# Optimization experiments

Measured on AMD Instinct MI355X. Metric: run time of the kernel, lower is better.

The kernel has to match this reference:

```python
import jax, jax.numpy as jnp
import numpy as np
import math

# dims: batch, seq_len, d_model, heads, head_dim
B, L, DM, H, DH = 1, 4096, 1024, 16, 64
BS, W, MAXD, DFF = 64, 16, 256, 4096  # block_size, band width (blocks), max rel distance, ffn dim
NB = L // BS


def _static_layout():
    # Static block-sparse causal band layout: tgt block n attends to src blocks [n-W+1 .. n].
    # Mirrors construct_blocksparse_rel_ids: rel = tgt_pos - src_pos, pos ids start at 1
    # (0 reserved for padding), clamp rel<-1 -> -1, rel>max_distance -> max_distance, then +1.
    n = np.arange(NB)[:, None, None, None]
    w = np.arange(W)[None, :, None, None]
    i = np.arange(BS)[None, None, :, None]
    j = np.arange(BS)[None, None, None, :]
    src_blk = n - (W - 1) + w
    # valid: block exists; diagonal block (w==W-1) is causal within-block (j<=i)
    valid = (src_blk >= 0) & ((w < W - 1) | (j <= i))
    tgt_pos = n * BS + i + 1
    src_pos = np.clip(src_blk, 0, None) * BS + j + 1
    rel = np.clip(tgt_pos - src_pos, -1, MAXD) + 1
    rel = np.where(valid, rel, 0)  # masked positions get rel id 0 (as in masked_fill_)
    src_idx = np.clip(np.arange(NB)[:, None] - (W - 1) + np.arange(W)[None, :], 0, None)
    return jnp.asarray(rel), jnp.asarray(valid), jnp.asarray(src_idx)

REL_IDS, VALID, SRC_IDX = _static_layout()  # [NB,W,BS,BS], [NB,W,BS,BS], [NB,W]


def _ln(x, g, b):
    m = x.mean(-1, keepdims=True)
    v = ((x - m) ** 2).mean(-1, keepdims=True)
    return (x - m) * jax.lax.rsqrt(v + 1e-5) * g + b


def setup_inputs() -> dict:
    key = jax.random.key(0)
    ks = jax.random.split(key, 10)
    p = lambda k, shape: jax.random.normal(k, shape, jnp.float32) * 0.02
    return dict(
        x=jax.random.normal(ks[0], (B, L, DM), jnp.float32),
        Wq=p(ks[1], (DM, DM)), Wk=p(ks[2], (DM, DM)), Wv=p(ks[3], (DM, DM)),
        Wo=p(ks[4], (DM, DM)),
        rel_emb=p(ks[5], (MAXD + 2, H)),  # per-head relative position bias table
        ln1_g=jnp.ones((DM,), jnp.float32), ln1_b=jnp.zeros((DM,), jnp.float32),
        ln2_g=jnp.ones((DM,), jnp.float32), ln2_b=jnp.zeros((DM,), jnp.float32),
        W1=p(ks[6], (DM, DFF)), b1=jnp.zeros((DFF,), jnp.float32),
        W2=p(ks[7], (DFF, DM)), b2=jnp.zeros((DM,), jnp.float32),
    )


def reference(x, Wq, Wk, Wv, Wo, rel_emb, ln1_g, ln1_b, ln2_g, ln2_b, W1, b1, W2, b2):
    h = _ln(x, ln1_g, ln1_b)

    def heads(Wt):
        return (h @ Wt).reshape(B, NB, BS, H, DH).transpose(0, 3, 1, 2, 4)  # [B,H,NB,BS,DH]

    q, k, v = heads(Wq), heads(Wk), heads(Wv)
    k_band = k[:, :, SRC_IDX]  # gather nonzero src blocks -> [B,H,NB,W,BS,DH]
    v_band = v[:, :, SRC_IDX]
    scores = jnp.einsum('bhnid,bhnwjd->bhniwj', q, k_band) / math.sqrt(DH)
    # relative position bias, per block pair and head
    bias = rel_emb[REL_IDS].transpose(4, 0, 2, 1, 3)  # [H,NB,BS,W,BS]
    scores = scores + bias[None]
    mask = VALID.transpose(0, 2, 1, 3)  # [NB,BS,W,BS]
    scores = jnp.where(mask, scores, jnp.float32(-1e30))
    p = jax.nn.softmax(scores.reshape(B, H, NB, BS, W * BS), axis=-1)
    p = p.reshape(B, H, NB, BS, W, BS)
    o = jnp.einsum('bhniwj,bhnwjd->bhnid', p, v_band)
    o = o.transpose(0, 2, 3, 1, 4).reshape(B, L, DM) @ Wo
    x = x + o
    h2 = _ln(x, ln2_g, ln2_b)
    x = x + (jax.nn.gelu(h2 @ W1 + b1) @ W2 + b2)
    return x
```

## Files before the change

kernel.cpp:

```cpp
#include <hip/hip_runtime.h>
#include <math.h>

typedef __bf16 bf16x8 __attribute__((ext_vector_type(8)));
typedef float  f32x4  __attribute__((ext_vector_type(4)));
typedef short  s16x8  __attribute__((ext_vector_type(8)));

__device__ __forceinline__ unsigned short f2bf(float f) {
    unsigned int u = __float_as_uint(f);
    u += 0x7fffu + ((u >> 16) & 1u);
    return (unsigned short)(u >> 16);
}

__device__ __forceinline__ float gelu_tanh(float x) {
    float x3 = x * x * x;
    float t = tanhf(0.7978845608028654f * (x + 0.044715f * x3));
    return 0.5f * x * (1.0f + t);
}

__global__ __launch_bounds__(256) void tcvt_kernel(const float* __restrict__ in,
                                                   unsigned short* __restrict__ out,
                                                   int K, int N) {
    __shared__ float tile[32][33];
    int tx = threadIdx.x, ty = threadIdx.y;
    int k0 = blockIdx.y * 32, n0 = blockIdx.x * 32;
#pragma unroll
    for (int s = 0; s < 4; ++s)
        tile[ty + s * 8][tx] = in[(size_t)(k0 + ty + s * 8) * N + n0 + tx];
    __syncthreads();
#pragma unroll
    for (int s = 0; s < 4; ++s)
        out[(size_t)(n0 + ty + s * 8) * K + k0 + tx] = f2bf(tile[tx][ty + s * 8]);
}

__global__ __launch_bounds__(256) void ln_kernel(const float* __restrict__ x,
                                                 const float* __restrict__ g,
                                                 const float* __restrict__ b,
                                                 unsigned short* __restrict__ out) {
    int row = blockIdx.x;
    int tid = threadIdx.x;
    float4 v = ((const float4*)(x + (size_t)row * 1024))[tid];
    float s  = v.x + v.y + v.z + v.w;
    float ss = v.x * v.x + v.y * v.y + v.z * v.z + v.w * v.w;
#pragma unroll
    for (int o = 32; o > 0; o >>= 1) { s += __shfl_down(s, o); ss += __shfl_down(ss, o); }
    __shared__ float red[8];
    if ((tid & 63) == 0) { red[(tid >> 6) * 2] = s; red[(tid >> 6) * 2 + 1] = ss; }
    __syncthreads();
    s  = red[0] + red[2] + red[4] + red[6];
    ss = red[1] + red[3] + red[5] + red[7];
    float mean = s * (1.0f / 1024.0f);
    float var  = ss * (1.0f / 1024.0f) - mean * mean;
    float rs   = rsqrtf(var + 1e-5f);
    float4 gv = ((const float4*)g)[tid];
    float4 bv = ((const float4*)b)[tid];
    ushort4 o4;
    o4.x = f2bf((v.x - mean) * rs * gv.x + bv.x);
    o4.y = f2bf((v.y - mean) * rs * gv.y + bv.y);
    o4.z = f2bf((v.z - mean) * rs * gv.z + bv.z);
    o4.w = f2bf((v.w - mean) * rs * gv.w + bv.w);
    ((ushort4*)(out + (size_t)row * 1024))[tid] = o4;
}

__global__ __launch_bounds__(256) void tvt_kernel(const unsigned short* __restrict__ in,
                                                  unsigned short* __restrict__ out) {
    __shared__ unsigned short tile[64][72];
    int t = threadIdx.x;
    int l0 = blockIdx.x * 64, c0 = blockIdx.y * 64;
    int tr = t >> 3, tc = (t & 7) * 8;
#pragma unroll
    for (int s = 0; s < 2; ++s) {
        int r = tr + s * 32;
        s16x8 v = *(const s16x8*)(in + (size_t)(l0 + r) * 3072 + 2048 + c0 + tc);
        *(s16x8*)(&tile[r][tc]) = v;
    }
    __syncthreads();
#pragma unroll
    for (int s = 0; s < 2; ++s) {
        int c = tr + s * 32;
        s16x8 w;
#pragma unroll
        for (int e = 0; e < 8; ++e) w[e] = (short)tile[tc + e][c];
        *(s16x8*)(out + (size_t)(c0 + c) * 4096 + l0 + tc) = w;
    }
}

#define BM 128
#define BN 128
#define BKK 64

template <int EPI>
__global__ __launch_bounds__(256) void gemm_kernel(const unsigned short* __restrict__ A,
                                                   const unsigned short* __restrict__ Bt,
                                                   void* __restrict__ C,
                                                   const float* __restrict__ bias,
                                                   const float* __restrict__ resid,
                                                   int M, int N, int K) {
    __shared__ __align__(16) unsigned short sA[BM * BKK];
    __shared__ __align__(16) unsigned short sB[BN * BKK];

    const int tid  = threadIdx.x;
    const int wv   = tid >> 6;
    const int lane = tid & 63;
    const int wr   = wv >> 1, wc = wv & 1;
    const int lg   = lane >> 4;
    const int l15  = lane & 15;

    const int brow = blockIdx.y * BM;
    const int bcol = blockIdx.x * BN;

    f32x4 acc[4][4] = {};

    const int l8 = lane >> 3;
    const int lc = (lane & 7) * 8;

    for (int kt = 0; kt < K; kt += BKK) {
        __syncthreads();
#pragma unroll
        for (int q = 0; q < 4; ++q) {
            int ch = 4 * wv + q;
            const unsigned short* srcA = A + (size_t)(brow + 8 * ch + l8) * K + kt + lc;
            __builtin_amdgcn_global_load_lds((const __attribute__((address_space(1))) void*)srcA,
                                             (__attribute__((address_space(3))) void*)(sA + ch * 512),
                                             16, 0, 0);
        }
#pragma unroll
        for (int q = 0; q < 4; ++q) {
            int ch = 4 * wv + q;
            const unsigned short* srcB = Bt + (size_t)(bcol + 8 * ch + l8) * K + kt + lc;
            __builtin_amdgcn_global_load_lds((const __attribute__((address_space(1))) void*)srcB,
                                             (__attribute__((address_space(3))) void*)(sB + ch * 512),
                                             16, 0, 0);
        }
        __syncthreads();

        bf16x8 af[4][2], bfr[4][2];
#pragma unroll
        for (int mi = 0; mi < 4; ++mi)
#pragma unroll
            for (int kk = 0; kk < 2; ++kk)
                af[mi][kk] = *(const bf16x8*)(sA + (wr * 64 + mi * 16 + l15) * BKK + lg * 8 + kk * 32);
#pragma unroll
        for (int ni = 0; ni < 4; ++ni)
#pragma unroll
            for (int kk = 0; kk < 2; ++kk)
                bfr[ni][kk] = *(const bf16x8*)(sB + (wc * 64 + ni * 16 + l15) * BKK + lg * 8 + kk * 32);

#pragma unroll
        for (int kk = 0; kk < 2; ++kk)
#pragma unroll
            for (int mi = 0; mi < 4; ++mi)
#pragma unroll
                for (int ni = 0; ni < 4; ++ni)
                    acc[mi][ni] = __builtin_amdgcn_mfma_f32_16x16x32_bf16(af[mi][kk], bfr[ni][kk],
                                                                          acc[mi][ni], 0, 0, 0);
    }

#pragma unroll
    for (int mi = 0; mi < 4; ++mi)
#pragma unroll
        for (int ni = 0; ni < 4; ++ni)
#pragma unroll
            for (int r = 0; r < 4; ++r) {
                int row = brow + wr * 64 + mi * 16 + lg * 4 + r;
                int col = bcol + wc * 64 + ni * 16 + l15;
                size_t idx = (size_t)row * N + col;
                float v = acc[mi][ni][r];
                if (EPI == 0) {
                    ((unsigned short*)C)[idx] = f2bf(v);
                } else if (EPI == 1) {
                    ((float*)C)[idx] = v + resid[idx];
                } else if (EPI == 2) {
                    v += bias[col];
                    ((unsigned short*)C)[idx] = f2bf(gelu_tanh(v));
                } else {
                    ((float*)C)[idx] = v + bias[col] + resid[idx];
                }
            }
}


__device__ __forceinline__ void stage64(const unsigned short* __restrict__ mat, int ld,
                                        int grow0, int kcol,
                                        unsigned short* lds_tile, int q, int wave, int lane) {
    const int l8 = lane >> 3;
    const int sc = ((lane & 7) ^ l8) << 3;
    const unsigned short* src = mat + (size_t)(grow0 + q * 64 + wave * 8 + l8) * ld + kcol + sc;
    unsigned short* dst = lds_tile + ((q * 64 + wave * 8) << 6);
    __builtin_amdgcn_global_load_lds((const __attribute__((address_space(1))) void*)src,
                                     (__attribute__((address_space(3))) void*)dst, 16, 0, 0);
}

__device__ __forceinline__ bf16x8 ldfrag(const unsigned short* tile, int row, int chunk) {
    return *(const bf16x8*)(tile + (row << 6) + ((chunk ^ (row & 7)) << 3));
}

template <int EPI>
__global__ __launch_bounds__(512, 2) void gemm256_kernel(
        const unsigned short* __restrict__ A, int lda,
        const unsigned short* __restrict__ Bt, int ldb,
        void* __restrict__ Cv, const float* __restrict__ bias,
        int ldc, int NT, int gm, int gn, unsigned long long slab_stride) {
    extern __shared__ unsigned short lds[];
    unsigned short* sA = lds;
    unsigned short* sB = lds + 2 * 256 * 64;

    const int tid  = threadIdx.x;
    const int wave = tid >> 6, lane = tid & 63;
    const int wr = wave >> 2, wc = wave & 3;
    const int lg = lane >> 4, l15 = lane & 15;

    const int nwg = gridDim.x;
    const int bid = blockIdx.x;
    const int q8 = nwg >> 3, r8 = nwg & 7;
    const int xcd = bid & 7, loc = bid >> 3;
    const int swz = (xcd < r8 ? xcd * (q8 + 1) : r8 * (q8 + 1) + (xcd - r8) * q8) + loc;
    const int split = swz / (gm * gn);
    const int rem   = swz % (gm * gn);
    const int brow = (rem / gn) << 8;
    const int bcol = (rem % gn) << 8;
    const int kbase = split * (NT << 6);

    f32x4 acc[8][4] = {};

#define STAGE_A(tt, q_, pbuf) stage64(A, lda, brow, kbase + ((tt) << 6), sA + (pbuf) * 16384, (q_), wave, lane)
#define STAGE_B(tt, q_, pbuf) stage64(Bt, ldb, bcol, kbase + ((tt) << 6), sB + (pbuf) * 16384, (q_), wave, lane)

    STAGE_A(0, 0, 0); STAGE_A(0, 1, 0); STAGE_A(0, 2, 0); STAGE_A(0, 3, 0);
    STAGE_B(0, 0, 0); STAGE_B(0, 1, 0); STAGE_B(0, 2, 0); STAGE_B(0, 3, 0);
    STAGE_A(1, 0, 1); STAGE_A(1, 1, 1); STAGE_A(1, 2, 1); STAGE_A(1, 3, 1);
    STAGE_B(1, 0, 1); STAGE_B(1, 1, 1);
    asm volatile("s_waitcnt vmcnt(6)" ::: "memory");
    __builtin_amdgcn_s_barrier();

    for (int t = 0; t < NT; ++t) {
        const int p = t & 1;
        const unsigned short* tA = sA + p * 16384;
        const unsigned short* tB = sB + p * 16384;
        bf16x8 a0[4][2], a1[4][2], b0[2][2], b1[2][2];

#pragma unroll
        for (int im = 0; im < 4; ++im)
#pragma unroll
            for (int kk = 0; kk < 2; ++kk)
                a0[im][kk] = ldfrag(tA, wr * 128 + im * 16 + l15, lg + kk * 4);
#pragma unroll
        for (int in = 0; in < 2; ++in)
#pragma unroll
            for (int kk = 0; kk < 2; ++kk)
                b0[in][kk] = ldfrag(tB, wc * 64 + in * 16 + l15, lg + kk * 4);
        if (t + 1 < NT) { STAGE_B(t + 1, 2, p ^ 1); STAGE_B(t + 1, 3, p ^ 1); }
        __builtin_amdgcn_s_barrier();
        asm volatile("s_waitcnt lgkmcnt(0)" ::: "memory");
        __builtin_amdgcn_sched_barrier(0);
        __builtin_amdgcn_s_setprio(1);
#pragma unroll
        for (int kk = 0; kk < 2; ++kk)
#pragma unroll
            for (int im = 0; im < 4; ++im)
#pragma unroll
                for (int in = 0; in < 2; ++in)
                    acc[im][in] = __builtin_amdgcn_mfma_f32_16x16x32_bf16(a0[im][kk], b0[in][kk], acc[im][in], 0, 0, 0);
        __builtin_amdgcn_s_setprio(0);
        __builtin_amdgcn_s_barrier();

#pragma unroll
        for (int im = 0; im < 4; ++im)
#pragma unroll
            for (int kk = 0; kk < 2; ++kk)
                a1[im][kk] = ldfrag(tA, wr * 128 + 64 + im * 16 + l15, lg + kk * 4);
        if (t + 2 < NT) { STAGE_A(t + 2, 0, p); STAGE_A(t + 2, 2, p); }
        __builtin_amdgcn_s_barrier();
        asm volatile("s_waitcnt lgkmcnt(0)" ::: "memory");
        __builtin_amdgcn_sched_barrier(0);
        __builtin_amdgcn_s_setprio(1);
#pragma unroll
        for (int kk = 0; kk < 2; ++kk)
#pragma unroll
            for (int im = 0; im < 4; ++im)
#pragma unroll
                for (int in = 0; in < 2; ++in)
                    acc[4 + im][in] = __builtin_amdgcn_mfma_f32_16x16x32_bf16(a1[im][kk], b0[in][kk], acc[4 + im][in], 0, 0, 0);
        __builtin_amdgcn_s_setprio(0);
        __builtin_amdgcn_s_barrier();

#pragma unroll
        for (int in = 0; in < 2; ++in)
#pragma unroll
            for (int kk = 0; kk < 2; ++kk)
                b1[in][kk] = ldfrag(tB, wc * 64 + 32 + in * 16 + l15, lg + kk * 4);
        if (t + 2 < NT) { STAGE_A(t + 2, 1, p); STAGE_A(t + 2, 3, p); }
        __builtin_amdgcn_s_barrier();
        asm volatile("s_waitcnt lgkmcnt(0)" ::: "memory");
        __builtin_amdgcn_sched_barrier(0);
        __builtin_amdgcn_s_setprio(1);
#pragma unroll
        for (int kk = 0; kk < 2; ++kk)
#pragma unroll
            for (int im = 0; im < 4; ++im)
#pragma unroll
                for (int in = 0; in < 2; ++in)
                    acc[4 + im][2 + in] = __builtin_amdgcn_mfma_f32_16x16x32_bf16(a1[im][kk], b1[in][kk], acc[4 + im][2 + in], 0, 0, 0);
        __builtin_amdgcn_s_setprio(0);
        __builtin_amdgcn_s_barrier();

        if (t + 2 < NT) { STAGE_B(t + 2, 0, p); STAGE_B(t + 2, 1, p); }
        __builtin_amdgcn_s_barrier();
        asm volatile("s_waitcnt lgkmcnt(0)" ::: "memory");
        __builtin_amdgcn_sched_barrier(0);
        __builtin_amdgcn_s_setprio(1);
#pragma unroll
        for (int kk = 0; kk < 2; ++kk)
#pragma unroll
            for (int im = 0; im < 4; ++im)
#pragma unroll
                for (int in = 0; in < 2; ++in)
                    acc[im][2 + in] = __builtin_amdgcn_mfma_f32_16x16x32_bf16(a0[im][kk], b1[in][kk], acc[im][2 + in], 0, 0, 0);
        __builtin_amdgcn_s_setprio(0);
        if (t + 2 < NT) asm volatile("s_waitcnt vmcnt(6)" ::: "memory");
        else            asm volatile("s_waitcnt vmcnt(0)" ::: "memory");
        __builtin_amdgcn_s_barrier();
    }
#undef STAGE_A
#undef STAGE_B

#pragma unroll
    for (int mi = 0; mi < 8; ++mi)
#pragma unroll
        for (int ni = 0; ni < 4; ++ni)
#pragma unroll
            for (int rr = 0; rr < 4; ++rr) {
                int row = brow + wr * 128 + mi * 16 + lg * 4 + rr;
                int col = bcol + wc * 64 + ni * 16 + l15;
                float v = acc[mi][ni][rr];
                if (EPI == 0) {
                    ((unsigned short*)Cv)[(size_t)row * ldc + col] = f2bf(v);
                } else if (EPI == 2) {
                    v += bias[col];
                    ((unsigned short*)Cv)[(size_t)row * ldc + col] = f2bf(gelu_tanh(v));
                } else {
                    ((unsigned short*)Cv)[slab_stride * split + (size_t)row * ldc + col] = f2bf(v);
                }
            }
}

__global__ __launch_bounds__(256) void reduce4_kernel(const unsigned short* __restrict__ part,
                                                      const float* __restrict__ bias,
                                                      const float* __restrict__ resid,
                                                      float* __restrict__ out) {
    int i4 = blockIdx.x * 256 + threadIdx.x;
    float4 r  = ((const float4*)resid)[i4];
    float4 bb = ((const float4*)bias)[i4 & 255];
    float s0 = r.x + bb.x, s1 = r.y + bb.y, s2 = r.z + bb.z, s3 = r.w + bb.w;
#pragma unroll
    for (int s = 0; s < 4; ++s) {
        ushort4 u = ((const ushort4*)(part + (size_t)s * 4194304))[i4];
        s0 += __uint_as_float((unsigned)u.x << 16);
        s1 += __uint_as_float((unsigned)u.y << 16);
        s2 += __uint_as_float((unsigned)u.z << 16);
        s3 += __uint_as_float((unsigned)u.w << 16);
    }
    float4 o; o.x = s0; o.y = s1; o.z = s2; o.w = s3;
    ((float4*)out)[i4] = o;
}

__global__ __launch_bounds__(256) void attn_kernel(const unsigned short* __restrict__ qkv,
                                                   const unsigned short* __restrict__ vt,
                                                   const float* __restrict__ rel_emb,
                                                   unsigned short* __restrict__ outp) {
    const int n = blockIdx.x;
    const int h = blockIdx.y;
    const int tid  = threadIdx.x;
    const int wv   = tid >> 6;
    const int lane = tid & 63;
    const int lg   = lane >> 4;
    const int l15  = lane & 15;

    __shared__ __align__(16) unsigned short sQ[64 * 72];
    __shared__ __align__(16) unsigned short sK[64 * 72];
    __shared__ __align__(16) unsigned short sV[64 * 72];
    __shared__ __align__(16) unsigned short sP[64 * 72];
    __shared__ float sRel[258];

    for (int i = tid; i < 258; i += 256) sRel[i] = rel_emb[i * 16 + h];

    {
        int tr = tid >> 3, tc = (tid & 7) * 8;
#pragma unroll
        for (int s = 0; s < 2; ++s) {
            int r = tr + s * 32;
            s16x8 v = *(const s16x8*)(qkv + (size_t)(n * 64 + r) * 3072 + h * 64 + tc);
            *(s16x8*)(&sQ[r * 72 + tc]) = v;
        }
    }
    __syncthreads();

    bf16x8 qf[2];
#pragma unroll
    for (int kk = 0; kk < 2; ++kk)
        qf[kk] = *(const bf16x8*)(sQ + (wv * 16 + l15) * 72 + lg * 8 + kk * 32);

    f32x4 oacc[4] = {};
    float mrow[4] = {-1e30f, -1e30f, -1e30f, -1e30f};
    float lrow[4] = {0.f, 0.f, 0.f, 0.f};

    const int w0 = (n >= 15) ? 0 : (15 - n);
    for (int w = w0; w < 16; ++w) {
        const int src = n - 15 + w;
        __syncthreads();
        {
            int tr = tid >> 3, tc = (tid & 7) * 8;
#pragma unroll
            for (int s = 0; s < 2; ++s) {
                int r = tr + s * 32;
                s16x8 kv = *(const s16x8*)(qkv + (size_t)(src * 64 + r) * 3072 + 1024 + h * 64 + tc);
                *(s16x8*)(&sK[r * 72 + tc]) = kv;
                s16x8 vv = *(const s16x8*)(vt + (size_t)(h * 64 + r) * 4096 + src * 64 + tc);
                *(s16x8*)(&sV[r * 72 + tc]) = vv;
            }
        }
        __syncthreads();

        f32x4 s[4] = {};
#pragma unroll
        for (int t = 0; t < 4; ++t)
#pragma unroll
            for (int kk = 0; kk < 2; ++kk) {
                bf16x8 kf = *(const bf16x8*)(sK + (t * 16 + l15) * 72 + lg * 8 + kk * 32);
                s[t] = __builtin_amdgcn_mfma_f32_16x16x32_bf16(qf[kk], kf, s[t], 0, 0, 0);
            }

        float pmax[4] = {-1e30f, -1e30f, -1e30f, -1e30f};
#pragma unroll
        for (int t = 0; t < 4; ++t)
#pragma unroll
            for (int r = 0; r < 4; ++r) {
                int i = wv * 16 + lg * 4 + r;
                int j = t * 16 + l15;
                float val;
                if (w < 15 || j <= i) {
                    int delta = (15 - w) * 64 + i - j;
                    int relid = min(delta, 256) + 1;
                    val = s[t][r] * 0.125f + sRel[relid];
                } else {
                    val = -1e30f;
                }
                s[t][r] = val;
                pmax[r] = fmaxf(pmax[r], val);
            }
#pragma unroll
        for (int r = 0; r < 4; ++r) {
#pragma unroll
            for (int m = 1; m < 16; m <<= 1) pmax[r] = fmaxf(pmax[r], __shfl_xor(pmax[r], m));
        }

        float scl[4], mnew[4];
#pragma unroll
        for (int r = 0; r < 4; ++r) {
            mnew[r] = fmaxf(mrow[r], pmax[r]);
            scl[r]  = __expf(mrow[r] - mnew[r]);
            mrow[r] = mnew[r];
        }

        float rsum[4] = {0.f, 0.f, 0.f, 0.f};
#pragma unroll
        for (int t = 0; t < 4; ++t)
#pragma unroll
            for (int r = 0; r < 4; ++r) {
                float p = __expf(s[t][r] - mnew[r]);
                rsum[r] += p;
                sP[(wv * 16 + lg * 4 + r) * 72 + t * 16 + l15] = f2bf(p);
            }
#pragma unroll
        for (int r = 0; r < 4; ++r) {
#pragma unroll
            for (int m = 1; m < 16; m <<= 1) rsum[r] += __shfl_xor(rsum[r], m);
            lrow[r] = lrow[r] * scl[r] + rsum[r];
        }
#pragma unroll
        for (int t = 0; t < 4; ++t)
#pragma unroll
            for (int r = 0; r < 4; ++r) oacc[t][r] *= scl[r];

        __syncthreads();

#pragma unroll
        for (int kk = 0; kk < 2; ++kk) {
            bf16x8 pf = *(const bf16x8*)(sP + (wv * 16 + l15) * 72 + lg * 8 + kk * 32);
#pragma unroll
            for (int t = 0; t < 4; ++t) {
                bf16x8 vf = *(const bf16x8*)(sV + (t * 16 + l15) * 72 + lg * 8 + kk * 32);
                oacc[t] = __builtin_amdgcn_mfma_f32_16x16x32_bf16(pf, vf, oacc[t], 0, 0, 0);
            }
        }
    }

#pragma unroll
    for (int t = 0; t < 4; ++t)
#pragma unroll
        for (int r = 0; r < 4; ++r) {
            float inv = 1.0f / lrow[r];
            size_t idx = (size_t)(n * 64 + wv * 16 + lg * 4 + r) * 1024 + h * 64 + t * 16 + l15;
            outp[idx] = f2bf(oacc[t][r] * inv);
        }
}

extern "C" void kernel_launch(void* const* d_in, const int* in_sizes, int n_in,
                              void* d_out, int out_size, void* d_ws, size_t ws_size,
                              hipStream_t stream) {
    const float* x    = (const float*)d_in[0];
    const float* Wq   = (const float*)d_in[1];
    const float* Wk   = (const float*)d_in[2];
    const float* Wv   = (const float*)d_in[3];
    const float* Wo   = (const float*)d_in[4];
    const float* rel  = (const float*)d_in[5];
    const float* ln1g = (const float*)d_in[6];
    const float* ln1b = (const float*)d_in[7];
    const float* ln2g = (const float*)d_in[8];
    const float* ln2b = (const float*)d_in[9];
    const float* W1   = (const float*)d_in[10];
    const float* b1   = (const float*)d_in[11];
    const float* W2   = (const float*)d_in[12];
    const float* b2   = (const float*)d_in[13];

    char* ws = (char*)d_ws;
    unsigned short* wqkvT = (unsigned short*)(ws + 0);
    unsigned short* woT   = (unsigned short*)(ws + 6291456);
    unsigned short* attnb = (unsigned short*)(ws + 8388608);
    unsigned short* w1T   = (unsigned short*)(ws + 16777216);
    unsigned short* hbuf  = (unsigned short*)(ws + 25165824);
    unsigned short* w2T   = (unsigned short*)(ws + 33554432);
    float*          x2    = (float*)(ws + 41943040);
    unsigned short* qkv   = (unsigned short*)(ws + 58720256);
    unsigned short* vt    = (unsigned short*)(ws + 83886080);
    unsigned short* gbuf  = (unsigned short*)(ws + 58720256);
    unsigned short* part  = (unsigned short*)(ws + 0);

    const int smem = 131072;
    hipFuncSetAttribute((const void*)gemm256_kernel<0>, hipFuncAttributeMaxDynamicSharedMemorySize, smem);
    hipFuncSetAttribute((const void*)gemm256_kernel<2>, hipFuncAttributeMaxDynamicSharedMemorySize, smem);
    hipFuncSetAttribute((const void*)gemm256_kernel<4>, hipFuncAttributeMaxDynamicSharedMemorySize, smem);

    dim3 tb(32, 8);
    tcvt_kernel<<<dim3(32, 32), tb, 0, stream>>>(Wq, wqkvT, 1024, 1024);
    tcvt_kernel<<<dim3(32, 32), tb, 0, stream>>>(Wk, wqkvT + 1048576, 1024, 1024);
    tcvt_kernel<<<dim3(32, 32), tb, 0, stream>>>(Wv, wqkvT + 2097152, 1024, 1024);
    tcvt_kernel<<<dim3(32, 32), tb, 0, stream>>>(Wo, woT, 1024, 1024);
    tcvt_kernel<<<dim3(128, 32), tb, 0, stream>>>(W1, w1T, 1024, 4096);
    tcvt_kernel<<<dim3(32, 128), tb, 0, stream>>>(W2, w2T, 4096, 1024);

    ln_kernel<<<4096, 256, 0, stream>>>(x, ln1g, ln1b, hbuf);

    gemm256_kernel<0><<<192, 512, smem, stream>>>(hbuf, 1024, wqkvT, 1024, qkv,
                                                  nullptr, 3072, 16, 16, 12, 0ULL);

    tvt_kernel<<<dim3(64, 16), 256, 0, stream>>>(qkv, vt);

    attn_kernel<<<dim3(64, 16), 256, 0, stream>>>(qkv, vt, rel, attnb);

    gemm_kernel<1><<<dim3(1024 / 128, 4096 / 128), 256, 0, stream>>>(attnb, woT, x2,
                                                                     nullptr, x, 4096, 1024, 1024);

    ln_kernel<<<4096, 256, 0, stream>>>(x2, ln2g, ln2b, hbuf);

    gemm256_kernel<2><<<256, 512, smem, stream>>>(hbuf, 1024, w1T, 1024, gbuf,
                                                  b1, 4096, 16, 16, 16, 0ULL);

    gemm256_kernel<4><<<256, 512, smem, stream>>>(gbuf, 4096, w2T, 4096, part,
                                                  nullptr, 1024, 16, 16, 4, 4194304ULL);

    reduce4_kernel<<<4096, 256, 0, stream>>>(part, b2, x2, (float*)d_out);
}
```

Measured before the change: 274.9 us.

## Restructure banded attention to share K/V across query-block pairs with double buffering

The attention kernel now handles two adjacent query blocks per workgroup. The K/V tiles for the 17 source blocks are loaded once, through asynchronous global-to-LDS copies into a double buffer, and shared between both query blocks, with each wave computing 32 query rows. It also specialises the relative-bias path (a constant bias for distant blocks, table lookups near the diagonal), reorders the grid by head for locality, and drops padding in favour of XOR-swizzled LDS. The cost is more registers per wave, hand-placed waitcnt/barrier synchronisation, and some waves idling at the band edges.

```diff
diff --git a/kernel.cpp b/kernel.cpp
--- a/kernel.cpp
+++ b/kernel.cpp
@@ -178,7 +178,6 @@
             }
 }
 
-
 __device__ __forceinline__ void stage64(const unsigned short* __restrict__ mat, int ld,
                                         int grow0, int kcol,
                                         unsigned short* lds_tile, int q, int wave, int lane) {
@@ -191,7 +190,7 @@
 }
 
 __device__ __forceinline__ bf16x8 ldfrag(const unsigned short* tile, int row, int chunk) {
-    return *(const bf16x8*)(tile + (row << 6) + ((chunk ^ (row & 7)) << 3));
+    return *(const bf16x8*)(tile + (row << 6) + (((chunk ^ row) & 7) << 3));
 }
 
 template <int EPI>
@@ -363,144 +362,236 @@
     ((float4*)out)[i4] = o;
 }
 
-__global__ __launch_bounds__(256) void attn_kernel(const unsigned short* __restrict__ qkv,
-                                                   const unsigned short* __restrict__ vt,
-                                                   const float* __restrict__ rel_emb,
-                                                   unsigned short* __restrict__ outp) {
-    const int n = blockIdx.x;
-    const int h = blockIdx.y;
+__device__ __forceinline__ void stage8(const unsigned short* __restrict__ src_row0, int ld,
+                                       unsigned short* ldsdst, int lane) {
+    const int r8 = lane >> 3;
+    const int c  = (lane & 7) ^ r8;
+    const unsigned short* src = src_row0 + (size_t)r8 * ld + c * 8;
+    __builtin_amdgcn_global_load_lds((const __attribute__((address_space(1))) void*)src,
+                                     (__attribute__((address_space(3))) void*)ldsdst, 16, 0, 0);
+}
+
+__global__ __launch_bounds__(256, 2) void attn2_kernel(const unsigned short* __restrict__ qkv,
+                                                       const unsigned short* __restrict__ vt,
+                                                       const float* __restrict__ rel_emb,
+                                                       unsigned short* __restrict__ outp) {
+    const int lid   = blockIdx.y * gridDim.x + blockIdx.x;
+    const int rid   = (lid & 7) * 64 + (lid >> 3);
+    const int h     = rid >> 5;
+    const int strip = rid & 31;
+    const int n0    = strip * 2;
+
     const int tid  = threadIdx.x;
     const int wv   = tid >> 6;
     const int lane = tid & 63;
+    const int qb   = wv >> 1;
+    const int half = wv & 1;
     const int lg   = lane >> 4;
     const int l15  = lane & 15;
-
-    __shared__ __align__(16) unsigned short sQ[64 * 72];
-    __shared__ __align__(16) unsigned short sK[64 * 72];
-    __shared__ __align__(16) unsigned short sV[64 * 72];
-    __shared__ __align__(16) unsigned short sP[64 * 72];
-    __shared__ float sRel[258];
-
-    for (int i = tid; i < 258; i += 256) sRel[i] = rel_emb[i * 16 + h];
-
+    const int nq   = n0 + qb;
+
+    __shared__ __align__(16) unsigned short sK[2][4096];
+    __shared__ __align__(16) unsigned short sV[2][4096];
+    __shared__ __align__(16) unsigned short sP[4][2048];
+    __shared__ float sRelF[258];
+
+    unsigned short* sQ  = &sP[0][0];
+    unsigned short* sPw = &sP[wv][0];
+
+    for (int i = tid; i < 258; i += 256) sRelF[i] = rel_emb[i * 16 + h];
+    const float relC = rel_emb[257 * 16 + h];
+
+    const int tlo = (n0 >= 15) ? 0 : (15 - n0);
+
+#pragma unroll
+    for (int s = 0; s < 4; ++s) {
+        int r0 = wv * 32 + s * 8;
+        stage8(qkv + (size_t)(n0 * 64 + r0) * 3072 + h * 64, 3072, sQ + r0 * 64, lane);
+    }
     {
-        int tr = tid >> 3, tc = (tid & 7) * 8;
+        const int src = n0 - 15 + tlo;
 #pragma unroll
         for (int s = 0; s < 2; ++s) {
-            int r = tr + s * 32;
-            s16x8 v = *(const s16x8*)(qkv + (size_t)(n * 64 + r) * 3072 + h * 64 + tc);
-            *(s16x8*)(&sQ[r * 72 + tc]) = v;
+            int r0 = wv * 16 + s * 8;
+            stage8(qkv + (size_t)(src * 64 + r0) * 3072 + 1024 + h * 64, 3072, &sK[0][r0 * 64], lane);
+            stage8(vt + (size_t)(h * 64 + r0) * 4096 + src * 64, 4096, &sV[0][r0 * 64], lane);
         }
     }
-    __syncthreads();
-
-    bf16x8 qf[2];
-#pragma unroll
-    for (int kk = 0; kk < 2; ++kk)
-        qf[kk] = *(const bf16x8*)(sQ + (wv * 16 + l15) * 72 + lg * 8 + kk * 32);
-
-    f32x4 oacc[4] = {};
-    float mrow[4] = {-1e30f, -1e30f, -1e30f, -1e30f};
-    float lrow[4] = {0.f, 0.f, 0.f, 0.f};
-
-    const int w0 = (n >= 15) ? 0 : (15 - n);
-    for (int w = w0; w < 16; ++w) {
-        const int src = n - 15 + w;
-        __syncthreads();
-        {
-            int tr = tid >> 3, tc = (tid & 7) * 8;
+    asm volatile("s_waitcnt vmcnt(4)" ::: "memory");
+    __builtin_amdgcn_s_barrier();
+
+    bf16x8 qf[2][2];
+#pragma unroll
+    for (int mi = 0; mi < 2; ++mi)
+#pragma unroll
+        for (int kk = 0; kk < 2; ++kk)
+            qf[mi][kk] = ldfrag(sQ, qb * 64 + half * 32 + mi * 16 + l15, lg + kk * 4);
+    asm volatile("s_waitcnt lgkmcnt(0)" ::: "memory");
+    __builtin_amdgcn_sched_barrier(0);
+    __builtin_amdgcn_s_barrier();
+
+    f32x4 oacc[2][4] = {};
+    float mrow[2][4], lrow[2][4];
+#pragma unroll
+    for (int mi = 0; mi < 2; ++mi)
+#pragma unroll
+        for (int rr = 0; rr < 4; ++rr) { mrow[mi][rr] = -1e30f; lrow[mi][rr] = 0.f; }
+
+    for (int t = tlo; t <= 16; ++t) {
+        const int cur = (t - tlo) & 1;
+        if (t < 16) {
+            const int src = n0 - 15 + (t + 1);
 #pragma unroll
             for (int s = 0; s < 2; ++s) {
-                int r = tr + s * 32;
-                s16x8 kv = *(const s16x8*)(qkv + (size_t)(src * 64 + r) * 3072 + 1024 + h * 64 + tc);
-                *(s16x8*)(&sK[r * 72 + tc]) = kv;
-                s16x8 vv = *(const s16x8*)(vt + (size_t)(h * 64 + r) * 4096 + src * 64 + tc);
-                *(s16x8*)(&sV[r * 72 + tc]) = vv;
+                int r0 = wv * 16 + s * 8;
+                stage8(qkv + (size_t)(src * 64 + r0) * 3072 + 1024 + h * 64, 3072, &sK[cur ^ 1][r0 * 64], lane);
+                stage8(vt + (size_t)(h * 64 + r0) * 4096 + src * 64, 4096, &sV[cur ^ 1][r0 * 64], lane);
             }
+            asm volatile("s_waitcnt vmcnt(4)" ::: "memory");
+        } else {
+            asm volatile("s_waitcnt vmcnt(0)" ::: "memory");
         }
-        __syncthreads();
-
-        f32x4 s[4] = {};
-#pragma unroll
-        for (int t = 0; t < 4; ++t)
-#pragma unroll
-            for (int kk = 0; kk < 2; ++kk) {
-                bf16x8 kf = *(const bf16x8*)(sK + (t * 16 + l15) * 72 + lg * 8 + kk * 32);
-                s[t] = __builtin_amdgcn_mfma_f32_16x16x32_bf16(qf[kk], kf, s[t], 0, 0, 0);
+        __builtin_amdgcn_s_barrier();
+
+        const bool act = (t >= qb) && (t - qb <= 15);
+        if (act) {
+            const unsigned short* tK = &sK[cur][0];
+            const unsigned short* tV = &sV[cur][0];
+            const int woff = 15 + qb - t;
+
+            f32x4 s[2][4] = {};
+            __builtin_amdgcn_s_setprio(1);
+#pragma unroll
+            for (int jt = 0; jt < 4; ++jt) {
+                bf16x8 kf0 = ldfrag(tK, jt * 16 + l15, lg);
+                bf16x8 kf1 = ldfrag(tK, jt * 16 + l15, lg + 4);
+#pragma unroll
+                for (int mi = 0; mi < 2; ++mi) {
+                    s[mi][jt] = __builtin_amdgcn_mfma_f32_16x16x32_bf16(qf[mi][0], kf0, s[mi][jt], 0, 0, 0);
+                    s[mi][jt] = __builtin_amdgcn_mfma_f32_16x16x32_bf16(qf[mi][1], kf1, s[mi][jt], 0, 0, 0);
+                }
             }
-
-        float pmax[4] = {-1e30f, -1e30f, -1e30f, -1e30f};
-#pragma unroll
-        for (int t = 0; t < 4; ++t)
-#pragma unroll
-            for (int r = 0; r < 4; ++r) {
-                int i = wv * 16 + lg * 4 + r;
-                int j = t * 16 + l15;
-                float val;
-                if (w < 15 || j <= i) {
-                    int delta = (15 - w) * 64 + i - j;
-                    int relid = min(delta, 256) + 1;
-                    val = s[t][r] * 0.125f + sRel[relid];
-                } else {
-                    val = -1e30f;
+            __builtin_amdgcn_s_setprio(0);
+
+            float pm[2][4];
+#pragma unroll
+            for (int mi = 0; mi < 2; ++mi)
+#pragma unroll
+                for (int rr = 0; rr < 4; ++rr) pm[mi][rr] = -1e30f;
+
+            if (woff >= 5) {
+#pragma unroll
+                for (int mi = 0; mi < 2; ++mi)
+#pragma unroll
+                    for (int jt = 0; jt < 4; ++jt)
+#pragma unroll
+                        for (int rr = 0; rr < 4; ++rr) {
+                            float v = s[mi][jt][rr] * 0.125f + relC;
+                            s[mi][jt][rr] = v;
+                            pm[mi][rr] = fmaxf(pm[mi][rr], v);
+                        }
+            } else if (woff > 0) {
+#pragma unroll
+                for (int mi = 0; mi < 2; ++mi)
+#pragma unroll
+                    for (int jt = 0; jt < 4; ++jt)
+#pragma unroll
+                        for (int rr = 0; rr < 4; ++rr) {
+                            int i = half * 32 + mi * 16 + lg * 4 + rr;
+                            int j = jt * 16 + l15;
+                            int relid = min(woff * 64 + i - j, 256) + 1;
+                            float v = s[mi][jt][rr] * 0.125f + sRelF[relid];
+                            s[mi][jt][rr] = v;
+                            pm[mi][rr] = fmaxf(pm[mi][rr], v);
+                        }
+            } else {
+#pragma unroll
+                for (int mi = 0; mi < 2; ++mi)
+#pragma unroll
+                    for (int jt = 0; jt < 4; ++jt)
+#pragma unroll
+                        for (int rr = 0; rr < 4; ++rr) {
+                            int i = half * 32 + mi * 16 + lg * 4 + rr;
+                            int j = jt * 16 + l15;
+                            float v = (j <= i) ? (s[mi][jt][rr] * 0.125f + sRelF[i - j + 1]) : -1e30f;
+                            s[mi][jt][rr] = v;
+                            pm[mi][rr] = fmaxf(pm[mi][rr], v);
+                        }
+            }
+
+            float scl[2][4], rs[2][4];
+#pragma unroll
+            for (int mi = 0; mi < 2; ++mi)
+#pragma unroll
+                for (int rr = 0; rr < 4; ++rr) {
+                    float v = pm[mi][rr];
+                    v = fmaxf(v, __shfl_xor(v, 1)); v = fmaxf(v, __shfl_xor(v, 2));
+                    v = fmaxf(v, __shfl_xor(v, 4)); v = fmaxf(v, __shfl_xor(v, 8));
+                    float mn = fmaxf(mrow[mi][rr], v);
+                    scl[mi][rr] = __expf(mrow[mi][rr] - mn);
+                    mrow[mi][rr] = mn;
+                    rs[mi][rr] = 0.f;
                 }
-                s[t][r] = val;
-                pmax[r] = fmaxf(pmax[r], val);
+#pragma unroll
+            for (int mi = 0; mi < 2; ++mi)
+#pragma unroll
+                for (int jt = 0; jt < 4; ++jt)
+#pragma unroll
+                    for (int rr = 0; rr < 4; ++rr) {
+                        float p = __expf(s[mi][jt][rr] - mrow[mi][rr]);
+                        rs[mi][rr] += p;
+                        int row = mi * 16 + lg * 4 + rr, col = jt * 16 + l15;
+                        sPw[(row << 6) + ((((col >> 3) ^ row) & 7) << 3) + (col & 7)] = f2bf(p);
+                    }
+#pragma unroll
+            for (int mi = 0; mi < 2; ++mi)
+#pragma unroll
+                for (int rr = 0; rr < 4; ++rr) {
+                    float v = rs[mi][rr];
+                    v += __shfl_xor(v, 1); v += __shfl_xor(v, 2);
+                    v += __shfl_xor(v, 4); v += __shfl_xor(v, 8);
+                    lrow[mi][rr] = lrow[mi][rr] * scl[mi][rr] + v;
+                }
+#pragma unroll
+            for (int mi = 0; mi < 2; ++mi)
+#pragma unroll
+                for (int dt = 0; dt < 4; ++dt)
+#pragma unroll
+                    for (int rr = 0; rr < 4; ++rr)
+                        oacc[mi][dt][rr] *= scl[mi][rr];
+
+            bf16x8 pf[2][2];
+#pragma unroll
+            for (int mi = 0; mi < 2; ++mi)
+#pragma unroll
+                for (int kk = 0; kk < 2; ++kk)
+                    pf[mi][kk] = ldfrag(sPw, mi * 16 + l15, lg + kk * 4);
+            __builtin_amdgcn_s_setprio(1);
+#pragma unroll
+            for (int dt = 0; dt < 4; ++dt) {
+                bf16x8 vf0 = ldfrag(tV, dt * 16 + l15, lg);
+                bf16x8 vf1 = ldfrag(tV, dt * 16 + l15, lg + 4);
+#pragma unroll
+                for (int mi = 0; mi < 2; ++mi) {
+                    oacc[mi][dt] = __builtin_amdgcn_mfma_f32_16x16x32_bf16(pf[mi][0], vf0, oacc[mi][dt], 0, 0, 0);
+                    oacc[mi][dt] = __builtin_amdgcn_mfma_f32_16x16x32_bf16(pf[mi][1], vf1, oacc[mi][dt], 0, 0, 0);
+                }
             }
-#pragma unroll
-        for (int r = 0; r < 4; ++r) {
-#pragma unroll
-            for (int m = 1; m < 16; m <<= 1) pmax[r] = fmaxf(pmax[r], __shfl_xor(pmax[r], m));
+            __builtin_amdgcn_s_setprio(0);
         }
-
-        float scl[4], mnew[4];
-#pragma unroll
-        for (int r = 0; r < 4; ++r) {
-            mnew[r] = fmaxf(mrow[r], pmax[r]);
-            scl[r]  = __expf(mrow[r] - mnew[r]);
-            mrow[r] = mnew[r];
-        }
-
-        float rsum[4] = {0.f, 0.f, 0.f, 0.f};
-#pragma unroll
-        for (int t = 0; t < 4; ++t)
-#pragma unroll
-            for (int r = 0; r < 4; ++r) {
-                float p = __expf(s[t][r] - mnew[r]);
-                rsum[r] += p;
-                sP[(wv * 16 + lg * 4 + r) * 72 + t * 16 + l15] = f2bf(p);
+        __builtin_amdgcn_s_barrier();
+    }
+
+#pragma unroll
+    for (int mi = 0; mi < 2; ++mi)
+#pragma unroll
+        for (int rr = 0; rr < 4; ++rr) {
+            float inv = 1.0f / lrow[mi][rr];
+#pragma unroll
+            for (int dt = 0; dt < 4; ++dt) {
+                size_t row = (size_t)(nq * 64 + half * 32 + mi * 16 + lg * 4 + rr);
+                outp[row * 1024 + h * 64 + dt * 16 + l15] = f2bf(oacc[mi][dt][rr] * inv);
             }
-#pragma unroll
-        for (int r = 0; r < 4; ++r) {
-#pragma unroll
-            for (int m = 1; m < 16; m <<= 1) rsum[r] += __shfl_xor(rsum[r], m);
-            lrow[r] = lrow[r] * scl[r] + rsum[r];
-        }
-#pragma unroll
-        for (int t = 0; t < 4; ++t)
-#pragma unroll
-            for (int r = 0; r < 4; ++r) oacc[t][r] *= scl[r];
-
-        __syncthreads();
-
-#pragma unroll
-        for (int kk = 0; kk < 2; ++kk) {
-            bf16x8 pf = *(const bf16x8*)(sP + (wv * 16 + l15) * 72 + lg * 8 + kk * 32);
-#pragma unroll
-            for (int t = 0; t < 4; ++t) {
-                bf16x8 vf = *(const bf16x8*)(sV + (t * 16 + l15) * 72 + lg * 8 + kk * 32);
-                oacc[t] = __builtin_amdgcn_mfma_f32_16x16x32_bf16(pf, vf, oacc[t], 0, 0, 0);
-            }
-        }
-    }
-
-#pragma unroll
-    for (int t = 0; t < 4; ++t)
-#pragma unroll
-        for (int r = 0; r < 4; ++r) {
-            float inv = 1.0f / lrow[r];
-            size_t idx = (size_t)(n * 64 + wv * 16 + lg * 4 + r) * 1024 + h * 64 + t * 16 + l15;
-            outp[idx] = f2bf(oacc[t][r] * inv);
         }
 }
 
@@ -555,7 +646,7 @@
 
     tvt_kernel<<<dim3(64, 16), 256, 0, stream>>>(qkv, vt);
 
-    attn_kernel<<<dim3(64, 16), 256, 0, stream>>>(qkv, vt, rel, attnb);
+    attn2_kernel<<<dim3(32, 16), 256, 0, stream>>>(qkv, vt, rel, attnb);
 
     gemm_kernel<1><<<dim3(1024 / 128, 4096 / 128), 256, 0, stream>>>(attnb, woT, x2,
                                                                      nullptr, x, 4096, 1024, 1024);
```

Result: faster. 263.1 us (-4.3%).
